# Kernel tuning notes

Hardware: AMD Instinct MI355X
Metric: run time of the kernel (lower is better)

Reference implementation:

```python
import jax, jax.numpy as jnp
import numpy as np

NUM_EMBEDDINGS = 1024
EMBEDDING_DIM = 64
BETA = 0.25


def setup_inputs() -> dict:
    key = jax.random.key(0)
    k1, k2 = jax.random.split(key)
    z = jax.random.normal(k1, (64, 32, 32, EMBEDDING_DIM), dtype=jnp.float32)
    emb = jax.random.uniform(
        k2, (NUM_EMBEDDINGS, EMBEDDING_DIM), dtype=jnp.float32,
        minval=-1.0 / NUM_EMBEDDINGS, maxval=1.0 / NUM_EMBEDDINGS)
    return {"z": z, "emb": emb}


def reference(z, emb):
    zf = z.reshape(-1, EMBEDDING_DIM)                      # [N, D]
    # squared L2 distances via ||z||^2 - 2 z.e + ||e||^2  -> [N, K]
    distances = (jnp.sum(zf * zf, axis=1, keepdims=True)
                 - 2.0 * jnp.matmul(zf, emb.T)
                 + jnp.sum(emb * emb, axis=1))
    encoding_indices = jnp.argmin(distances, axis=1)       # [N]
    quantized = emb[encoding_indices].reshape(z.shape)     # [B, H, W, D]
    commitment_loss = BETA * jnp.mean((jax.lax.stop_gradient(quantized) - z) ** 2)
    codebook_loss = jnp.mean((quantized - jax.lax.stop_gradient(z)) ** 2)
    loss = commitment_loss + codebook_loss
    # straight-through estimator
    quantized = z + jax.lax.stop_gradient(quantized - z)
    return (quantized, loss)
```

## Files before the change

kernel.cpp:

```cpp
#include <hip/hip_runtime.h>
#include <stdint.h>

#define N_ROWS 65536
#define K_CODES 1024
#define D 64
#define OUT_ELEMS 4194304
#define LOSS_SCALE (1.25f / 4194304.0f)
#define ROWS_PER_BLOCK 256
#define GRID_DIST (N_ROWS / ROWS_PER_BLOCK)

typedef short short8 __attribute__((ext_vector_type(8)));
typedef float f32x4 __attribute__((ext_vector_type(4)));

__device__ __forceinline__ unsigned short f2bf(float f) {
    unsigned int u = __float_as_uint(f);
    return (unsigned short)((u + 0x7fffu + ((u >> 16) & 1u)) >> 16);
}

#define GLOAD_LDS16(g, l)                                                          \
    __builtin_amdgcn_global_load_lds((const __attribute__((address_space(1))) void*)(g), \
                                     (__attribute__((address_space(3))) void*)(l), 16, 0, 0)

#define ECH (K_CODES * D / 8)
__global__ __launch_bounds__(256) void prep_kernel(const float* __restrict__ emb,
                                                   unsigned short* __restrict__ ebm2,
                                                   float* __restrict__ e2) {
    int t = blockIdx.x * 256 + threadIdx.x;
    if (t < ECH) {
        const float4* s = (const float4*)emb;
        float4 a = s[2 * t], b = s[2 * t + 1];
        uint4 o;
        o.x = f2bf(-2.f * a.x) | ((unsigned int)f2bf(-2.f * a.y) << 16);
        o.y = f2bf(-2.f * a.z) | ((unsigned int)f2bf(-2.f * a.w) << 16);
        o.z = f2bf(-2.f * b.x) | ((unsigned int)f2bf(-2.f * b.y) << 16);
        o.w = f2bf(-2.f * b.z) | ((unsigned int)f2bf(-2.f * b.w) << 16);
        ((uint4*)ebm2)[t] = o;
    } else if (t < ECH + K_CODES) {
        int k = t - ECH;
        const float4* e4 = (const float4*)emb;
        float s = 0.f;
#pragma unroll
        for (int i = 0; i < 16; i++) {
            float4 v = e4[k * 16 + i];
            s += v.x * v.x + v.y * v.y + v.z * v.z + v.w * v.w;
        }
        e2[k] = s;
    }
}

__global__ __launch_bounds__(256) void dist_fused_kernel(
        const float* __restrict__ z, const unsigned short* __restrict__ ebm2,
        const float* __restrict__ e2, const float* __restrict__ emb,
        float* __restrict__ out, float* __restrict__ partials) {
    __shared__ __align__(16) char smem[65536];
    const int tid = threadIdx.x;
    const int wave = tid >> 6, lane = tid & 63;
    const int n = lane & 15, q = lane >> 4, nb = n & 7;
    const int wave_row0 = blockIdx.x * ROWS_PER_BLOCK + wave * 64;

    auto stage = [&](int c) {
        const int bufoff = (c & 1) << 15;
        const uint4* gsrc = (const uint4*)ebm2;
#pragma unroll
        for (int r = 0; r < 8; r++) {
            int S = c * 2048 + r * 256 + tid;
            int P = (S & ~7) | ((S & 7) ^ ((S >> 3) & 7));
            char* l = smem + bufoff + (r * 256 + (tid & ~63)) * 16;
            GLOAD_LDS16(gsrc + P, l);
        }
    };
    stage(0);

    short8 b[4][2];
    float z2p[4];
#pragma unroll
    for (int rs = 0; rs < 4; rs++) {
        const float* zr = z + (size_t)(wave_row0 + rs * 16 + n) * D + q * 8;
        float4 f0 = *(const float4*)(zr);
        float4 f1 = *(const float4*)(zr + 4);
        float4 f2 = *(const float4*)(zr + 32);
        float4 f3 = *(const float4*)(zr + 36);
        z2p[rs] = f0.x*f0.x + f0.y*f0.y + f0.z*f0.z + f0.w*f0.w
                + f1.x*f1.x + f1.y*f1.y + f1.z*f1.z + f1.w*f1.w
                + f2.x*f2.x + f2.y*f2.y + f2.z*f2.z + f2.w*f2.w
                + f3.x*f3.x + f3.y*f3.y + f3.z*f3.z + f3.w*f3.w;
        short8 lo, hi;
        lo[0] = f2bf(f0.x); lo[1] = f2bf(f0.y); lo[2] = f2bf(f0.z); lo[3] = f2bf(f0.w);
        lo[4] = f2bf(f1.x); lo[5] = f2bf(f1.y); lo[6] = f2bf(f1.z); lo[7] = f2bf(f1.w);
        hi[0] = f2bf(f2.x); hi[1] = f2bf(f2.y); hi[2] = f2bf(f2.z); hi[3] = f2bf(f2.w);
        hi[4] = f2bf(f3.x); hi[5] = f2bf(f3.y); hi[6] = f2bf(f3.z); hi[7] = f2bf(f3.w);
        b[rs][0] = lo; b[rs][1] = hi;
    }

    f32x4 Ea = *(const f32x4*)(e2 + q * 4);
    f32x4 Eb = *(const f32x4*)(e2 + 16 + q * 4);
    const int base0 = n * 128 + ((q ^ nb) << 4);
    const int base1 = n * 128 + (((4 | q) ^ nb) << 4);

    float bestd[4] = {INFINITY, INFINITY, INFINITY, INFINITY};
    int bestk[4] = {0, 0, 0, 0};

    __syncthreads();
    for (int c = 0; c < 4; c++) {
        if (c < 3) stage(c + 1);
        const char* buf = smem + ((c & 1) << 15);
#pragma unroll
        for (int tl = 0; tl < 16; tl++) {
            const int t = c * 16 + tl;
            short8 a0 = *(const short8*)(buf + tl * 2048 + base0);
            short8 a1 = *(const short8*)(buf + tl * 2048 + base1);
            f32x4 E = (tl & 1) ? Eb : Ea;
            f32x4 acc[4];
#pragma unroll
            for (int rs = 0; rs < 4; rs++) {
                f32x4 a = E;
                a = __builtin_amdgcn_mfma_f32_16x16x32_bf16(a0, b[rs][0], a, 0, 0, 0);
                a = __builtin_amdgcn_mfma_f32_16x16x32_bf16(a1, b[rs][1], a, 0, 0, 0);
                acc[rs] = a;
            }
            int tp = (t + 2 > 63) ? 63 : (t + 2);
            f32x4 En = *(const f32x4*)(e2 + tp * 16 + q * 4);
            if (tl & 1) Eb = En; else Ea = En;
#pragma unroll
            for (int rs = 0; rs < 4; rs++)
#pragma unroll
                for (int r = 0; r < 4; r++) {
                    float d = acc[rs][r];
                    if (d < bestd[rs]) { bestd[rs] = d; bestk[rs] = t * 16 + q * 4 + r; }
                }
        }
        __syncthreads();
    }

    float lossl = 0.f;
    int bidx[4];
#pragma unroll
    for (int rs = 0; rs < 4; rs++) {
        unsigned int db = __float_as_uint(bestd[rs]);
        db = (db & 0x80000000u) ? ~db : (db | 0x80000000u);
        unsigned long long key = ((unsigned long long)db << 32) | (unsigned int)bestk[rs];
        unsigned long long o = __shfl_xor(key, 16, 64); key = o < key ? o : key;
        o = __shfl_xor(key, 32, 64); key = o < key ? o : key;
        bidx[rs] = (int)(key & 0xFFFFFFFFu);
        unsigned int eu = (unsigned int)(key >> 32);
        float bd = __uint_as_float((eu & 0x80000000u) ? (eu & 0x7FFFFFFFu) : ~eu);
        float z2r = z2p[rs];
        z2r += __shfl_xor(z2r, 16, 64);
        z2r += __shfl_xor(z2r, 32, 64);
        lossl += bd + z2r;
    }

    const float4* emb4 = (const float4*)emb;
    float4* o4 = (float4*)out + (size_t)wave_row0 * 16;
#pragma unroll
    for (int it = 0; it < 16; it++) {
        int k = __shfl(bidx[it >> 2], (it * 4 + q) & 15, 64);
        o4[it * 64 + lane] = emb4[k * 16 + n];
    }

#pragma unroll
    for (int off = 32; off > 0; off >>= 1)
        lossl += __shfl_down(lossl, off, 64);
    float* ps = (float*)smem;
    if (lane == 0) ps[wave] = lossl;
    __syncthreads();
    if (tid == 0) partials[blockIdx.x] = 0.25f * (ps[0] + ps[1] + ps[2] + ps[3]);
}

__global__ __launch_bounds__(256) void loss_kernel(const float* __restrict__ partials,
                                                   float* __restrict__ loss) {
    float s = partials[threadIdx.x];
#pragma unroll
    for (int off = 32; off > 0; off >>= 1)
        s += __shfl_down(s, off, 64);
    __shared__ float ps[4];
    int wave = threadIdx.x >> 6, lane = threadIdx.x & 63;
    if (lane == 0) ps[wave] = s;
    __syncthreads();
    if (threadIdx.x == 0) loss[0] = (ps[0] + ps[1] + ps[2] + ps[3]) * LOSS_SCALE;
}

extern "C" void kernel_launch(void* const* d_in, const int* in_sizes, int n_in,
                              void* d_out, int out_size, void* d_ws, size_t ws_size,
                              hipStream_t stream) {
    const float* z = (const float*)d_in[0];
    const float* emb = (const float*)d_in[1];
    float* out = (float*)d_out;
    float* loss = out + OUT_ELEMS;

    char* ws = (char*)d_ws;
    float* e2 = (float*)ws;
    unsigned short* ebm2 = (unsigned short*)(ws + 4096);
    float* partials = (float*)(ws + 4096 + 131072 + 8192);

    prep_kernel<<<(ECH + K_CODES + 255) / 256, 256, 0, stream>>>(emb, ebm2, e2);
    dist_fused_kernel<<<GRID_DIST, 256, 0, stream>>>(z, ebm2, e2, emb, out, partials);
    loss_kernel<<<1, 256, 0, stream>>>(partials, loss);
}
```

Before: 92.94 us.

## Stage whole codebook in LDS once and pack argmin into 32-bit keys

The whole bf16 codebook and the e2 norms are now loaded into 132KB of dynamic LDS up front, replacing the double-buffered chunk staging and the per-chunk barriers. ||z||^2 (plus 1.0 to keep distances positive) is folded into the MFMA accumulator init. The argmin becomes a single unsigned min over keys whose low 10 mantissa bits are replaced by the code index, which cuts compares and registers. The truncated-key argmin can pick a different index when two distances are very close. The large LDS allocation limits occupancy to one block per CU.

```diff
diff --git a/kernel.cpp b/kernel.cpp
--- a/kernel.cpp
+++ b/kernel.cpp
@@ -8,6 +8,7 @@
 #define LOSS_SCALE (1.25f / 4194304.0f)
 #define ROWS_PER_BLOCK 256
 #define GRID_DIST (N_ROWS / ROWS_PER_BLOCK)
+#define LDS_BYTES 135168
 
 typedef short short8 __attribute__((ext_vector_type(8)));
 typedef float f32x4 __attribute__((ext_vector_type(4)));
@@ -52,27 +53,26 @@
         const float* __restrict__ z, const unsigned short* __restrict__ ebm2,
         const float* __restrict__ e2, const float* __restrict__ emb,
         float* __restrict__ out, float* __restrict__ partials) {
-    __shared__ __align__(16) char smem[65536];
+    extern __shared__ __align__(16) char smem[];
     const int tid = threadIdx.x;
     const int wave = tid >> 6, lane = tid & 63;
     const int n = lane & 15, q = lane >> 4, nb = n & 7;
     const int wave_row0 = blockIdx.x * ROWS_PER_BLOCK + wave * 64;
 
-    auto stage = [&](int c) {
-        const int bufoff = (c & 1) << 15;
+    {
         const uint4* gsrc = (const uint4*)ebm2;
 #pragma unroll
-        for (int r = 0; r < 8; r++) {
-            int S = c * 2048 + r * 256 + tid;
+        for (int r = 0; r < 32; r++) {
+            int S = r * 256 + tid;
             int P = (S & ~7) | ((S & 7) ^ ((S >> 3) & 7));
-            char* l = smem + bufoff + (r * 256 + (tid & ~63)) * 16;
+            char* l = smem + (r * 256 + (tid & ~63)) * 16;
             GLOAD_LDS16(gsrc + P, l);
         }
-    };
-    stage(0);
+        GLOAD_LDS16(e2 + tid * 4, smem + 131072 + (tid & ~63) * 16);
+    }
 
     short8 b[4][2];
-    float z2p[4];
+    float z2c[4];
 #pragma unroll
     for (int rs = 0; rs < 4; rs++) {
         const float* zr = z + (size_t)(wave_row0 + rs * 16 + n) * D + q * 8;
@@ -80,10 +80,13 @@
         float4 f1 = *(const float4*)(zr + 4);
         float4 f2 = *(const float4*)(zr + 32);
         float4 f3 = *(const float4*)(zr + 36);
-        z2p[rs] = f0.x*f0.x + f0.y*f0.y + f0.z*f0.z + f0.w*f0.w
-                + f1.x*f1.x + f1.y*f1.y + f1.z*f1.z + f1.w*f1.w
-                + f2.x*f2.x + f2.y*f2.y + f2.z*f2.z + f2.w*f2.w
-                + f3.x*f3.x + f3.y*f3.y + f3.z*f3.z + f3.w*f3.w;
+        float z2p = f0.x*f0.x + f0.y*f0.y + f0.z*f0.z + f0.w*f0.w
+                  + f1.x*f1.x + f1.y*f1.y + f1.z*f1.z + f1.w*f1.w
+                  + f2.x*f2.x + f2.y*f2.y + f2.z*f2.z + f2.w*f2.w
+                  + f3.x*f3.x + f3.y*f3.y + f3.z*f3.z + f3.w*f3.w;
+        z2p += __shfl_xor(z2p, 16, 64);
+        z2p += __shfl_xor(z2p, 32, 64);
+        z2c[rs] = z2p + 1.0f;
         short8 lo, hi;
         lo[0] = f2bf(f0.x); lo[1] = f2bf(f0.y); lo[2] = f2bf(f0.z); lo[3] = f2bf(f0.w);
         lo[4] = f2bf(f1.x); lo[5] = f2bf(f1.y); lo[6] = f2bf(f1.z); lo[7] = f2bf(f1.w);
@@ -92,62 +95,47 @@
         b[rs][0] = lo; b[rs][1] = hi;
     }
 
-    f32x4 Ea = *(const f32x4*)(e2 + q * 4);
-    f32x4 Eb = *(const f32x4*)(e2 + 16 + q * 4);
     const int base0 = n * 128 + ((q ^ nb) << 4);
     const int base1 = n * 128 + (((4 | q) ^ nb) << 4);
-
-    float bestd[4] = {INFINITY, INFINITY, INFINITY, INFINITY};
-    int bestk[4] = {0, 0, 0, 0};
+    const int vq4 = q * 4;
+    unsigned int best[4] = {0xFFFFFFFFu, 0xFFFFFFFFu, 0xFFFFFFFFu, 0xFFFFFFFFu};
 
     __syncthreads();
+
     for (int c = 0; c < 4; c++) {
-        if (c < 3) stage(c + 1);
-        const char* buf = smem + ((c & 1) << 15);
+        const unsigned int kc = c * 256 + vq4;
 #pragma unroll
         for (int tl = 0; tl < 16; tl++) {
             const int t = c * 16 + tl;
-            short8 a0 = *(const short8*)(buf + tl * 2048 + base0);
-            short8 a1 = *(const short8*)(buf + tl * 2048 + base1);
-            f32x4 E = (tl & 1) ? Eb : Ea;
-            f32x4 acc[4];
+            short8 a0 = *(const short8*)(smem + t * 2048 + base0);
+            short8 a1 = *(const short8*)(smem + t * 2048 + base1);
+            f32x4 E = *(const f32x4*)(smem + 131072 + t * 64 + vq4 * 4);
+            const unsigned int k0i = kc + tl * 16;
 #pragma unroll
             for (int rs = 0; rs < 4; rs++) {
-                f32x4 a = E;
+                f32x4 a = E + z2c[rs];
                 a = __builtin_amdgcn_mfma_f32_16x16x32_bf16(a0, b[rs][0], a, 0, 0, 0);
                 a = __builtin_amdgcn_mfma_f32_16x16x32_bf16(a1, b[rs][1], a, 0, 0, 0);
-                acc[rs] = a;
-            }
-            int tp = (t + 2 > 63) ? 63 : (t + 2);
-            f32x4 En = *(const f32x4*)(e2 + tp * 16 + q * 4);
-            if (tl & 1) Eb = En; else Ea = En;
-#pragma unroll
-            for (int rs = 0; rs < 4; rs++)
 #pragma unroll
                 for (int r = 0; r < 4; r++) {
-                    float d = acc[rs][r];
-                    if (d < bestd[rs]) { bestd[rs] = d; bestk[rs] = t * 16 + q * 4 + r; }
+                    unsigned int key = (__float_as_uint(a[r]) & 0xFFFFFC00u) | (k0i + r);
+                    best[rs] = best[rs] < key ? best[rs] : key;
                 }
+            }
         }
-        __syncthreads();
     }
 
     float lossl = 0.f;
     int bidx[4];
 #pragma unroll
     for (int rs = 0; rs < 4; rs++) {
-        unsigned int db = __float_as_uint(bestd[rs]);
-        db = (db & 0x80000000u) ? ~db : (db | 0x80000000u);
-        unsigned long long key = ((unsigned long long)db << 32) | (unsigned int)bestk[rs];
-        unsigned long long o = __shfl_xor(key, 16, 64); key = o < key ? o : key;
-        o = __shfl_xor(key, 32, 64); key = o < key ? o : key;
-        bidx[rs] = (int)(key & 0xFFFFFFFFu);
-        unsigned int eu = (unsigned int)(key >> 32);
-        float bd = __uint_as_float((eu & 0x80000000u) ? (eu & 0x7FFFFFFFu) : ~eu);
-        float z2r = z2p[rs];
-        z2r += __shfl_xor(z2r, 16, 64);
-        z2r += __shfl_xor(z2r, 32, 64);
-        lossl += bd + z2r;
+        unsigned int key = best[rs];
+        unsigned int o = (unsigned int)__shfl_xor((int)key, 16, 64);
+        key = o < key ? o : key;
+        o = (unsigned int)__shfl_xor((int)key, 32, 64);
+        key = o < key ? o : key;
+        bidx[rs] = (int)(key & 1023u);
+        lossl += __uint_as_float(key & 0xFFFFFC00u) - 1.0f;
     }
 
     const float4* emb4 = (const float4*)emb;
@@ -161,6 +149,7 @@
 #pragma unroll
     for (int off = 32; off > 0; off >>= 1)
         lossl += __shfl_down(lossl, off, 64);
+    __syncthreads();
     float* ps = (float*)smem;
     if (lane == 0) ps[wave] = lossl;
     __syncthreads();
@@ -193,7 +182,10 @@
     unsigned short* ebm2 = (unsigned short*)(ws + 4096);
     float* partials = (float*)(ws + 4096 + 131072 + 8192);
 
+    hipFuncSetAttribute((const void*)dist_fused_kernel,
+                        hipFuncAttributeMaxDynamicSharedMemorySize, LDS_BYTES);
+
     prep_kernel<<<(ECH + K_CODES + 255) / 256, 256, 0, stream>>>(emb, ebm2, e2);
-    dist_fused_kernel<<<GRID_DIST, 256, 0, stream>>>(z, ebm2, e2, emb, out, partials);
+    dist_fused_kernel<<<GRID_DIST, 256, LDS_BYTES, stream>>>(z, ebm2, e2, emb, out, partials);
     loss_kernel<<<1, 256, 0, stream>>>(partials, loss);
 }
```

Result: slower. 98.47 us (+5.9%).
